# Kernel tuning notes

Measured on AMD Instinct MI355X. Metric: run time of the kernel, lower is better.

Reference implementation:

```python
import jax, jax.numpy as jnp
import numpy as np

BATCH = 1024
M = 64      # N_v measurements
N = 8192    # N_theta unknowns
STEPS = 3   # N_admm_steps
EPS_DIV = 1e-12


def setup_inputs() -> dict:
    key = jax.random.key(0)
    k = jax.random.split(key, 4)
    return {
        "r_n": jax.random.normal(k[0], (BATCH, 2, N), jnp.float32),
        "y": jax.random.normal(k[1], (BATCH, 2, M), jnp.float32),
        "u_in": jax.random.normal(k[2], (BATCH, 2, M), jnp.float32),
        "A": jax.random.normal(k[3], (2, M, N), jnp.float32) / np.sqrt(N).astype(np.float32),
        "log_rho": jnp.zeros((), jnp.float32),                 # rho = 1.0
        "log_epsilon": jnp.asarray(np.log(0.01), jnp.float32), # epsilon = 0.01
    }


def _cmm(Ar, Ai, v):
    # complex matmul A @ v : v [b,2,N] -> [b,2,M]
    vr, vi = v[:, 0], v[:, 1]
    return jnp.stack([vr @ Ar.T - vi @ Ai.T, vi @ Ar.T + vr @ Ai.T], axis=1)


def _chm(Ar, Ai, v):
    # complex conj-transpose matmul A^H @ v : v [b,2,M] -> [b,2,N]
    vr, vi = v[:, 0], v[:, 1]
    return jnp.stack([vr @ Ar + vi @ Ai, vi @ Ar - vr @ Ai], axis=1)


def reference(r_n, y, u_in, A, log_rho, log_epsilon):
    rho = jnp.exp(log_rho)
    epsilon = jnp.exp(log_epsilon)
    Ar, Ai = A[0], A[1]  # [M, N]

    # SMW system matrix: S = (1/rho) I + A A^H, written as real 2Mx2M block matrix.
    # It is constant across ADMM steps (rho fixed within a forward pass).
    I_M = jnp.eye(M, dtype=A.dtype)
    S_r = I_M / (rho + EPS_DIV) + Ar @ Ar.T + Ai @ Ai.T
    S_i = Ai @ Ar.T - Ar @ Ai.T
    S_block = jnp.block([[S_r, -S_i], [S_i, S_r]])  # [2M, 2M]

    x, z, u = r_n, y, u_in
    for _ in range(STEPS):
        # x-update via SMW: x = b - A^H (S^{-1} A b), b = r_n + rho A^H (z - u)
        b = r_n + rho * _chm(Ar, Ai, z - u)          # [b,2,N]
        Ab = _cmm(Ar, Ai, b)                          # [b,2,M]
        R = jnp.concatenate([Ab[:, 0], Ab[:, 1]], axis=1)  # [b,2M]
        sol = jnp.linalg.solve(S_block, R.T)          # [2M, b]
        T = jnp.stack([sol[:M].T, sol[M:].T], axis=1)  # [b,2,M]
        x = b - _chm(Ar, Ai, T)                       # [b,2,N]
        # enforce_real: zero imaginary part; enforce_positivity: clamp real part
        x = jnp.stack([jnp.maximum(x[:, 0], 0.0), jnp.zeros_like(x[:, 0])], axis=1)
        # z-update: project residual onto complex L2 ball of radius epsilon
        Ax = _cmm(Ar, Ai, x)                          # [b,2,M]
        v = Ax + u - y
        nrm = jnp.sqrt(jnp.sum(v * v, axis=(1, 2), keepdims=True))
        z = y + v * jnp.minimum(1.0, epsilon / (nrm + EPS_DIV))
        # dual update
        u = u + Ax - z
    return x, u
```

## Files before the change

kernel.cpp:

```cpp
#include <hip/hip_runtime.h>

#define B_ 1024
#define M_ 64
#define N_ 8192
#define NSG 16
#define NS3 8

typedef __attribute__((ext_vector_type(8))) short bf16x8;
typedef __attribute__((ext_vector_type(4))) float f32x4;

__device__ inline unsigned short f2b(float f) {
    union { float f; unsigned u; } v; v.f = f;
    unsigned r = v.u + 0x7FFFu + ((v.u >> 16) & 1u);
    return (unsigned short)(r >> 16);
}
__device__ inline unsigned rne2(float lo, float hi) {
    union { float f; unsigned u; } a, b; a.f = lo; b.f = hi;
    unsigned x = (a.u + 0x7FFFu + ((a.u >> 16) & 1u)) >> 16;
    unsigned y = (b.u + 0x7FFFu + ((b.u >> 16) & 1u)) >> 16;
    return x | (y << 16);
}
__device__ inline float b2f(unsigned short s) {
    union { unsigned u; float f; } v; v.u = ((unsigned)s) << 16; return v.f;
}
__device__ inline float rl(float v, int l) {
    return __builtin_bit_cast(float, __builtin_amdgcn_readlane(__builtin_bit_cast(int, v), l));
}

__global__ __launch_bounds__(256) void k_cvt(const float* src, unsigned short* dst) {
    size_t i = ((size_t)blockIdx.x * 256 + threadIdx.x) * 8;
    float4 f0 = *(const float4*)(src + i);
    float4 f1 = *(const float4*)(src + i + 4);
    union { bf16x8 v; unsigned u[4]; } r;
    r.u[0] = rne2(f0.x, f0.y); r.u[1] = rne2(f0.z, f0.w);
    r.u[2] = rne2(f1.x, f1.y); r.u[3] = rne2(f1.z, f1.w);
    *(bf16x8*)(dst + i) = r.v;
}

__global__ __launch_bounds__(256) void k_prep(const float* A, unsigned short* Abf,
                                              unsigned short* WgT, unsigned short* ATb) {
    __shared__ float tile[128][65];
    int n0 = blockIdx.x * 64;
    int t = threadIdx.x;
    int nl = t % 64, r0 = t / 64;
#pragma unroll
    for (int it = 0; it < 32; ++it) {
        int row = r0 + it * 4;
        tile[row][nl] = A[(size_t)row * N_ + n0 + nl];
    }
    __syncthreads();
#pragma unroll
    for (int it = 0; it < 32; ++it) {
        int row = r0 + it * 4;
        float v = tile[row][nl];
        unsigned short bv = f2b(v);
        Abf[(size_t)row * N_ + n0 + nl] = bv;
        if (row < 64) {
            WgT[(size_t)row * 16384 + n0 + nl] = bv;
            WgT[(size_t)(64 + row) * 16384 + 8192 + n0 + nl] = bv;
        } else {
            int m = row - 64;
            WgT[(size_t)m * 16384 + 8192 + n0 + nl] = f2b(-v);
            WgT[(size_t)(64 + m) * 16384 + n0 + nl] = bv;
        }
    }
    int o = t % 128, nn0 = t / 128;
#pragma unroll
    for (int it = 0; it < 32; ++it) {
        int nn = nn0 + it * 2;
        ATb[(size_t)(n0 + nn) * 128 + o] = f2b(tile[o][nn]);
    }
}

__global__ __launch_bounds__(256) void k_Sbuild(const float* A, const float* lr,
                                                float* S, float* AAHT) {
    __shared__ float redS[8];
    int bid = blockIdx.x;
    int i = 0, rem = bid;
    while (rem >= 64 - i) { rem -= 64 - i; ++i; }
    int j = i + rem;
    int t = threadIdx.x;
    const float* Ar = A;
    const float* Ai = A + (size_t)M_ * N_;
    const float* ari = Ar + (size_t)i * N_;
    const float* aii = Ai + (size_t)i * N_;
    const float* arj = Ar + (size_t)j * N_;
    const float* aij = Ai + (size_t)j * N_;
    float aR = 0.f, aI = 0.f;
#pragma unroll
    for (int it = 0; it < 8; ++it) {
        int n = it * 1024 + t * 4;
        float4 xr = *(const float4*)(ari + n);
        float4 xi = *(const float4*)(aii + n);
        float4 br = *(const float4*)(arj + n);
        float4 bi = *(const float4*)(aij + n);
        aR += xr.x * br.x + xi.x * bi.x + xr.y * br.y + xi.y * bi.y
            + xr.z * br.z + xi.z * bi.z + xr.w * br.w + xi.w * bi.w;
        aI += xi.x * br.x - xr.x * bi.x + xi.y * br.y - xr.y * bi.y
            + xi.z * br.z - xr.z * bi.z + xi.w * br.w - xr.w * bi.w;
    }
    for (int off = 32; off > 0; off >>= 1) {
        aR += __shfl_down(aR, off, 64);
        aI += __shfl_down(aI, off, 64);
    }
    int lane = t & 63, w = t >> 6;
    if (lane == 0) { redS[w * 2] = aR; redS[w * 2 + 1] = aI; }
    __syncthreads();
    if (t == 0) {
        float R = redS[0] + redS[2] + redS[4] + redS[6];
        float I = redS[1] + redS[3] + redS[5] + redS[7];
        float inv_rho = 1.0f / (expf(lr[0]) + 1e-12f);
        float diag = (i == j) ? inv_rho : 0.f;
        S[((size_t)i * 64 + j) * 2 + 0] = R + diag;
        S[((size_t)i * 64 + j) * 2 + 1] = I;
        AAHT[((size_t)j * 64 + i) * 2 + 0] = R;
        AAHT[((size_t)j * 64 + i) * 2 + 1] = I;
        if (i != j) {
            S[((size_t)j * 64 + i) * 2 + 0] = R;
            S[((size_t)j * 64 + i) * 2 + 1] = -I;
            AAHT[((size_t)i * 64 + j) * 2 + 0] = R;
            AAHT[((size_t)i * 64 + j) * 2 + 1] = -I;
        }
    }
}

__global__ __launch_bounds__(256, 2) void k_Ginv(const unsigned short* rnb,
                                                 const unsigned short* WgT,
                                                 float* Gpart,
                                                 const float* S, float* Wt) {
    int t = threadIdx.x;
    int lane = t & 63;
    if (blockIdx.x == 0) {
        __builtin_amdgcn_s_setprio(1);
        __shared__ float2 Tp[2][4][64];
        int g = t >> 6;
        float mx0,my0,mx1,my1,mx2,my2,mx3,my3,mx4,my4,mx5,my5,mx6,my6,mx7,my7;
        float mx8,my8,mx9,my9,mx10,my10,mx11,my11,mx12,my12,mx13,my13,mx14,my14,mx15,my15;
#define GJ_INIT(J) { int c = 16 * ((J) >> 2) + 4 * g + ((J) & 3);            \
    float2 v = ((const float2*)S)[(size_t)lane * 64 + c];                    \
    mx##J = v.x; my##J = v.y; }
        GJ_INIT(0) GJ_INIT(1) GJ_INIT(2) GJ_INIT(3) GJ_INIT(4) GJ_INIT(5) GJ_INIT(6) GJ_INIT(7)
        GJ_INIT(8) GJ_INIT(9) GJ_INIT(10) GJ_INIT(11) GJ_INIT(12) GJ_INIT(13) GJ_INIT(14) GJ_INIT(15)
#undef GJ_INIT

#define PIV(JA, JB0, JB1, JB2, jj) {                                         \
    int k = p4 + (jj);                                                       \
    float px = rl(mx##JA, k), py = rl(my##JA, k);                            \
    float d = px * px + py * py;                                             \
    float id = 1.0f / d;                                                     \
    float pix = px * id, piy = -py * id;                                     \
    bool isk = (lane == k);                                                  \
    float a   = isk ? 0.f : 1.f;                                             \
    float fpx = isk ? -pix : (mx##JA * pix - my##JA * piy);                  \
    float fpy = isk ? -piy : (mx##JA * piy + my##JA * pix);                  \
    { float sx = rl(mx##JB0, k), sy = rl(my##JB0, k);                        \
      float nx = a * mx##JB0 - (fpx * sx - fpy * sy);                        \
      float ny = a * my##JB0 - (fpx * sy + fpy * sx);                        \
      mx##JB0 = nx; my##JB0 = ny; }                                          \
    { float sx = rl(mx##JB1, k), sy = rl(my##JB1, k);                        \
      float nx = a * mx##JB1 - (fpx * sx - fpy * sy);                        \
      float ny = a * my##JB1 - (fpx * sy + fpy * sx);                        \
      mx##JB1 = nx; my##JB1 = ny; }                                          \
    { float sx = rl(mx##JB2, k), sy = rl(my##JB2, k);                        \
      float nx = a * mx##JB2 - (fpx * sx - fpy * sy);                        \
      float ny = a * my##JB2 - (fpx * sy + fpy * sx);                        \
      mx##JB2 = nx; my##JB2 = ny; }                                          \
    mx##JA = -fpx; my##JA = -fpy; }

#define FACT4(J0, J1, J2, J3) {                                              \
    PIV(J0, J1, J2, J3, 0) PIV(J1, J0, J2, J3, 1)                            \
    PIV(J2, J0, J1, J3, 2) PIV(J3, J0, J1, J2, 3)                            \
    Tp[buf][0][lane] = make_float2(mx##J0, my##J0);                          \
    Tp[buf][1][lane] = make_float2(mx##J1, my##J1);                          \
    Tp[buf][2][lane] = make_float2(mx##J2, my##J2);                          \
    Tp[buf][3][lane] = make_float2(mx##J3, my##J3); }

        for (int p = 0; p < 16; ++p) {
            const int buf = p & 1;
            const int p4  = p * 4;
            const int q   = p >> 2;
            const bool own = (g == (p & 3));
            if (own) {
                switch (q) {
                    case 0:  FACT4(0, 1, 2, 3)     break;
                    case 1:  FACT4(4, 5, 6, 7)     break;
                    case 2:  FACT4(8, 9, 10, 11)   break;
                    default: FACT4(12, 13, 14, 15) break;
                }
            }
            __syncthreads();
            float2 t0 = Tp[buf][0][lane];
            float2 t1 = Tp[buf][1][lane];
            float2 t2 = Tp[buf][2][lane];
            float2 t3 = Tp[buf][3][lane];
            float msk = ((lane >> 2) == p) ? 0.f : 1.f;
            int skipq = own ? q : -1;
#define TRAIL(J) if (((J) >> 2) != skipq) {                                  \
    float s0x = rl(mx##J, p4),     s0y = rl(my##J, p4);                      \
    float s1x = rl(mx##J, p4 + 1), s1y = rl(my##J, p4 + 1);                  \
    float s2x = rl(mx##J, p4 + 2), s2y = rl(my##J, p4 + 2);                  \
    float s3x = rl(mx##J, p4 + 3), s3y = rl(my##J, p4 + 3);                  \
    float ax = msk * mx##J, ay = msk * my##J;                                \
    ax += t0.x * s0x - t0.y * s0y; ay += t0.x * s0y + t0.y * s0x;            \
    ax += t1.x * s1x - t1.y * s1y; ay += t1.x * s1y + t1.y * s1x;            \
    ax += t2.x * s2x - t2.y * s2y; ay += t2.x * s2y + t2.y * s2x;            \
    ax += t3.x * s3x - t3.y * s3y; ay += t3.x * s3y + t3.y * s3x;            \
    mx##J = ax; my##J = ay; }
            TRAIL(0)  TRAIL(1)  TRAIL(2)  TRAIL(3)
            TRAIL(4)  TRAIL(5)  TRAIL(6)  TRAIL(7)
            TRAIL(8)  TRAIL(9)  TRAIL(10) TRAIL(11)
            TRAIL(12) TRAIL(13) TRAIL(14) TRAIL(15)
#undef TRAIL
        }
#undef FACT4
#undef PIV
#define GJ_OUT(J) { int c = 16 * ((J) >> 2) + 4 * g + ((J) & 3);             \
    ((float2*)Wt)[(size_t)c * 64 + lane] = make_float2(mx##J, my##J); }
        GJ_OUT(0) GJ_OUT(1) GJ_OUT(2) GJ_OUT(3) GJ_OUT(4) GJ_OUT(5) GJ_OUT(6) GJ_OUT(7)
        GJ_OUT(8) GJ_OUT(9) GJ_OUT(10) GJ_OUT(11) GJ_OUT(12) GJ_OUT(13) GJ_OUT(14) GJ_OUT(15)
#undef GJ_OUT
        __builtin_amdgcn_s_setprio(0);
    }
    int bx = blockIdx.x;
    int w = t >> 6;
    int l15 = lane & 15;
    int q8 = (lane >> 4) * 8;
    int split = bx & 15;
    int b0 = (bx >> 4) * 16;
    int k0 = split * 1024;
    f32x4 a00 = {}, a01 = {};
    const unsigned short* x0 = rnb + (size_t)(b0 + l15) * 16384 + k0 + q8;
    const unsigned short* w0 = WgT + (size_t)(w * 32 + l15) * 16384 + k0 + q8;
    const unsigned short* w1 = w0 + (size_t)16 * 16384;
#pragma unroll 8
    for (int ks = 0; ks < 32; ++ks) {
        int kk = ks * 32;
        bf16x8 af0 = *(const bf16x8*)(x0 + kk);
        bf16x8 bf0 = *(const bf16x8*)(w0 + kk);
        bf16x8 bf1 = *(const bf16x8*)(w1 + kk);
        a00 = __builtin_amdgcn_mfma_f32_16x16x32_bf16(af0, bf0, a00, 0, 0, 0);
        a01 = __builtin_amdgcn_mfma_f32_16x16x32_bf16(af0, bf1, a01, 0, 0, 0);
    }
    int row = (lane >> 4) * 4;
    size_t base = (size_t)split * (B_ * 128);
    float* g = Gpart + base + (size_t)(b0 + row) * 128 + w * 32 + l15;
#pragma unroll
    for (int r = 0; r < 4; ++r) {
        g[(size_t)r * 128] = a00[r];
        g[(size_t)r * 128 + 16] = a01[r];
    }
}

__global__ __launch_bounds__(256) void k_small12(const float* Gpart, const float* AAHT,
                                                 const float* Wt, const float* zin,
                                                 const float* uin, const float* lr,
                                                 unsigned short* qb) {
    __shared__ float2 AbS[4][64];
    int t = threadIdx.x;
    int m = t & 63;
    int w = __builtin_amdgcn_readfirstlane(t >> 6);
    int b = blockIdx.x * 4 + w;
    float rho = expf(lr[0]);
    float abR = 0.f, abI = 0.f;
    for (int k = 0; k < 64; ++k) {
        float wr = zin[(b * 2 + 0) * 64 + k] - uin[(b * 2 + 0) * 64 + k];
        float wi = zin[(b * 2 + 1) * 64 + k] - uin[(b * 2 + 1) * 64 + k];
        float2 h = *(const float2*)(AAHT + ((size_t)k * 64 + m) * 2);
        abR += wr * h.x - wi * h.y;
        abI += wi * h.x + wr * h.y;
    }
    float gR = 0.f, gI = 0.f;
#pragma unroll
    for (int s = 0; s < NSG; ++s) {
        gR += Gpart[(size_t)s * 131072 + (size_t)b * 128 + m];
        gI += Gpart[(size_t)s * 131072 + (size_t)b * 128 + 64 + m];
    }
    abR = gR + rho * abR;
    abI = gI + rho * abI;
    AbS[w][m] = make_float2(abR, abI);
    __syncthreads();
    float tR = 0.f, tI = 0.f;
    for (int k = 0; k < 64; ++k) {
        float2 Wv = *(const float2*)(Wt + ((size_t)k * 64 + m) * 2);
        float2 ab = AbS[w][k];
        tR += ab.x * Wv.x - ab.y * Wv.y;
        tI += ab.y * Wv.x + ab.x * Wv.y;
    }
    float wr_m = zin[(b * 2 + 0) * 64 + m] - uin[(b * 2 + 0) * 64 + m];
    float wi_m = zin[(b * 2 + 1) * 64 + m] - uin[(b * 2 + 1) * 64 + m];
    qb[(size_t)b * 128 + m] = f2b(rho * wr_m - tR);
    qb[(size_t)b * 128 + 64 + m] = f2b(rho * wi_m - tI);
}

__global__ __launch_bounds__(512, 2) void k_H23(const unsigned short* qb, const unsigned short* ATb,
                                                const unsigned short* rnb, const unsigned short* Abf,
                                                float* out, float* Axpart, int last) {
    __shared__ __align__(16) char lds_buf[8 * 8448];
    int t = threadIdx.x;
    int lane = t & 63;
    int w = t >> 6;
    int l15 = lane & 15;
    int q8 = (lane >> 4) * 8;
    int row = (lane >> 4) * 4;
    int slab = blockIdx.x;
    int b0 = blockIdx.y * 16;
    int n0 = slab * 1024 + w * 128;
    short* xs = (short*)(lds_buf + w * 8448);
    float* rs = (float*)(lds_buf + w * 8448);

    bf16x8 a[4];
    const unsigned short* qrow = qb + (size_t)(b0 + l15) * 128 + q8;
#pragma unroll
    for (int ks = 0; ks < 4; ++ks) a[ks] = *(const bf16x8*)(qrow + ks * 32);
#pragma unroll 2
    for (int nt = 0; nt < 8; ++nt) {
        f32x4 acc = {};
        const unsigned short* bbase = ATb + (size_t)(n0 + nt * 16 + l15) * 128 + q8;
#pragma unroll
        for (int ks = 0; ks < 4; ++ks) {
            bf16x8 bf = *(const bf16x8*)(bbase + ks * 32);
            acc = __builtin_amdgcn_mfma_f32_16x16x32_bf16(a[ks], bf, acc, 0, 0, 0);
        }
        int ncol = n0 + nt * 16 + l15;
        int nloc = nt * 16 + l15;
#pragma unroll
        for (int r = 0; r < 4; ++r) {
            size_t ridx = (size_t)(b0 + row + r) * 16384 + ncol;
            float v = fmaxf(acc[r] + b2f(rnb[ridx]), 0.f);
            if (last) out[ridx] = v;
            xs[(row + r) * 264 + nloc] = (short)f2b(v);
        }
    }
    f32x4 acc8[8] = {};
#pragma unroll
    for (int ks = 0; ks < 4; ++ks) {
        bf16x8 xf = *(const bf16x8*)(xs + l15 * 264 + ks * 32 + q8);
#pragma unroll
        for (int ot = 0; ot < 8; ++ot) {
            const unsigned short* bp = Abf + (size_t)(ot * 16 + l15) * 8192 + n0 + ks * 32 + q8;
            acc8[ot] = __builtin_amdgcn_mfma_f32_16x16x32_bf16(xf, *(const bf16x8*)bp, acc8[ot], 0, 0, 0);
        }
    }
    __syncthreads();
#pragma unroll
    for (int ot = 0; ot < 8; ++ot)
#pragma unroll
        for (int r = 0; r < 4; ++r)
            rs[(row + r) * 132 + ot * 16 + l15] = acc8[ot][r];
    __syncthreads();
#pragma unroll
    for (int e = t; e < 2048; e += 512) {
        int b = e >> 7, o = e & 127;
        float sAx = 0.f;
#pragma unroll
        for (int ww = 0; ww < 8; ++ww)
            sAx += ((const float*)(lds_buf + ww * 8448))[b * 132 + o];
        Axpart[(size_t)slab * 131072 + (size_t)(b0 + b) * 128 + o] = sAx;
    }
    if (last) {
        float4 z4 = make_float4(0.f, 0.f, 0.f, 0.f);
        for (int e = t; e < 4096; e += 512) {
            int bb = e >> 8, nq = e & 255;
            *(float4*)(out + ((size_t)(b0 + bb) * 2 + 1) * N_ + slab * 1024 + nq * 4) = z4;
        }
    }
}

__global__ __launch_bounds__(128) void k_small3(const float* Axpart, const float* uin,
                                                const float* y, const float* le,
                                                float* z, float* u, float* uout, int last) {
    __shared__ float red[2];
    int b = blockIdx.x, t = threadIdx.x;
    size_t idx = (size_t)b * 128 + t;
    float ax = 0.f;
#pragma unroll
    for (int s = 0; s < NS3; ++s) ax += Axpart[(size_t)s * 131072 + idx];
    float uo = uin[idx], yv = y[idx];
    float v = ax + uo - yv;
    float sq = v * v;
    for (int off = 32; off > 0; off >>= 1) sq += __shfl_down(sq, off, 64);
    if ((t & 63) == 0) red[t >> 6] = sq;
    __syncthreads();
    float tot = red[0] + red[1];
    float eps = expf(le[0]);
    float scale = fminf(1.f, eps / (sqrtf(tot) + 1e-12f));
    float zv = yv + v * scale;
    float un = uo + ax - zv;
    z[idx] = zv;
    u[idx] = un;
    if (last) uout[idx] = un;
}

extern "C" void kernel_launch(void* const* d_in, const int* in_sizes, int n_in,
                              void* d_out, int out_size, void* d_ws, size_t ws_size,
                              hipStream_t stream) {
    const float* rn  = (const float*)d_in[0];
    const float* y   = (const float*)d_in[1];
    const float* uin = (const float*)d_in[2];
    const float* A   = (const float*)d_in[3];
    const float* lr  = (const float*)d_in[4];
    const float* le  = (const float*)d_in[5];

    float* out = (float*)d_out;
    float* ws  = (float*)d_ws;

    float* Gpart  = ws;
    float* Axpart = Gpart + (size_t)NSG * 131072;
    float* S      = Axpart + (size_t)NS3 * 131072;
    float* AAHT   = S + 8192;
    float* Wt     = AAHT + 8192;
    float* z      = Wt + 8192;
    float* u      = z + 131072;
    unsigned short* qb  = (unsigned short*)(u + 131072);
    unsigned short* rnb = qb + 131072;
    unsigned short* WgT = rnb + (size_t)B_ * 16384;
    unsigned short* Abf = WgT + 2097152;
    unsigned short* ATb = Abf + 1048576;
    float* uout = out + (size_t)B_ * 2 * N_;

    k_prep<<<128, 256, 0, stream>>>(A, Abf, WgT, ATb);
    k_cvt<<<8192, 256, 0, stream>>>(rn, rnb);
    k_Sbuild<<<2080, 256, 0, stream>>>(A, lr, S, AAHT);
    k_Ginv<<<1024, 256, 0, stream>>>(rnb, WgT, Gpart, S, Wt);

    for (int step = 0; step < 3; ++step) {
        const float* zp = (step == 0) ? y   : z;
        const float* up = (step == 0) ? uin : u;
        int last = (step == 2) ? 1 : 0;
        k_small12<<<256, 256, 0, stream>>>(Gpart, AAHT, Wt, zp, up, lr, qb);
        k_H23<<<dim3(NS3, 64), 512, 0, stream>>>(qb, ATb, rnb, Abf, out, Axpart, last);
        k_small3<<<B_, 128, 0, stream>>>(Axpart, up, y, le, z, u, uout, last);
    }
}
```

Measured before the change: 341.1 us.

## Split small12 reductions across waves and move imag-zeroing into prep kernel

k_small12 now assigns one batch row per block and splits the 64-term k loops and Gpart split sums across four waves, combining partials through LDS. The aim is to cut the serial per-thread latency of that small kernel and raise parallelism. The zero-fill of the output's imaginary half moves out of the last k_H23 call into 2048 extra blocks of k_prep, so the final H23 no longer carries those stores. The cost is extra syncs and LDS traffic in small12, plus a larger prep launch.

```diff
diff --git a/kernel.cpp b/kernel.cpp
--- a/kernel.cpp
+++ b/kernel.cpp
@@ -38,7 +38,18 @@
 }
 
 __global__ __launch_bounds__(256) void k_prep(const float* A, unsigned short* Abf,
-                                              unsigned short* WgT, unsigned short* ATb) {
+                                              unsigned short* WgT, unsigned short* ATb,
+                                              float* out) {
+    if (blockIdx.x >= 128) {
+        int z = blockIdx.x - 128;
+        int fi = z * 4096 + threadIdx.x * 16;
+        int b = fi >> 13;
+        int n = fi & 8191;
+        float4* p = (float4*)(out + (size_t)b * 16384 + 8192 + n);
+        float4 z4 = make_float4(0.f, 0.f, 0.f, 0.f);
+        p[0] = z4; p[1] = z4; p[2] = z4; p[3] = z4;
+        return;
+    }
     __shared__ float tile[128][65];
     int n0 = blockIdx.x * 64;
     int t = threadIdx.x;
@@ -255,41 +266,58 @@
                                                  const float* Wt, const float* zin,
                                                  const float* uin, const float* lr,
                                                  unsigned short* qb) {
-    __shared__ float2 AbS[4][64];
+    __shared__ float2 partA[4][64];
+    __shared__ float2 partB[4][64];
+    __shared__ float2 AbS[64];
     int t = threadIdx.x;
     int m = t & 63;
     int w = __builtin_amdgcn_readfirstlane(t >> 6);
-    int b = blockIdx.x * 4 + w;
+    int b = blockIdx.x;
     float rho = expf(lr[0]);
-    float abR = 0.f, abI = 0.f;
-    for (int k = 0; k < 64; ++k) {
+    float aR = 0.f, aI = 0.f;
+#pragma unroll
+    for (int kk = 0; kk < 16; ++kk) {
+        int k = w * 16 + kk;
         float wr = zin[(b * 2 + 0) * 64 + k] - uin[(b * 2 + 0) * 64 + k];
         float wi = zin[(b * 2 + 1) * 64 + k] - uin[(b * 2 + 1) * 64 + k];
         float2 h = *(const float2*)(AAHT + ((size_t)k * 64 + m) * 2);
-        abR += wr * h.x - wi * h.y;
-        abI += wi * h.x + wr * h.y;
-    }
-    float gR = 0.f, gI = 0.f;
-#pragma unroll
-    for (int s = 0; s < NSG; ++s) {
-        gR += Gpart[(size_t)s * 131072 + (size_t)b * 128 + m];
-        gI += Gpart[(size_t)s * 131072 + (size_t)b * 128 + 64 + m];
-    }
-    abR = gR + rho * abR;
-    abI = gI + rho * abI;
-    AbS[w][m] = make_float2(abR, abI);
+        aR += wr * h.x - wi * h.y;
+        aI += wi * h.x + wr * h.y;
+    }
+    aR *= rho; aI *= rho;
+#pragma unroll
+    for (int s4 = 0; s4 < 4; ++s4) {
+        int s = w * 4 + s4;
+        aR += Gpart[(size_t)s * 131072 + (size_t)b * 128 + m];
+        aI += Gpart[(size_t)s * 131072 + (size_t)b * 128 + 64 + m];
+    }
+    partA[w][m] = make_float2(aR, aI);
+    __syncthreads();
+    if (w == 0) {
+        float2 p0 = partA[0][m], p1 = partA[1][m], p2 = partA[2][m], p3 = partA[3][m];
+        AbS[m] = make_float2(p0.x + p1.x + p2.x + p3.x, p0.y + p1.y + p2.y + p3.y);
+    }
     __syncthreads();
     float tR = 0.f, tI = 0.f;
-    for (int k = 0; k < 64; ++k) {
+#pragma unroll
+    for (int kk = 0; kk < 16; ++kk) {
+        int k = w * 16 + kk;
         float2 Wv = *(const float2*)(Wt + ((size_t)k * 64 + m) * 2);
-        float2 ab = AbS[w][k];
+        float2 ab = AbS[k];
         tR += ab.x * Wv.x - ab.y * Wv.y;
         tI += ab.y * Wv.x + ab.x * Wv.y;
     }
-    float wr_m = zin[(b * 2 + 0) * 64 + m] - uin[(b * 2 + 0) * 64 + m];
-    float wi_m = zin[(b * 2 + 1) * 64 + m] - uin[(b * 2 + 1) * 64 + m];
-    qb[(size_t)b * 128 + m] = f2b(rho * wr_m - tR);
-    qb[(size_t)b * 128 + 64 + m] = f2b(rho * wi_m - tI);
+    partB[w][m] = make_float2(tR, tI);
+    __syncthreads();
+    if (w == 0) {
+        float2 q0 = partB[0][m], q1 = partB[1][m], q2 = partB[2][m], q3 = partB[3][m];
+        float sR = q0.x + q1.x + q2.x + q3.x;
+        float sI = q0.y + q1.y + q2.y + q3.y;
+        float wr_m = zin[(b * 2 + 0) * 64 + m] - uin[(b * 2 + 0) * 64 + m];
+        float wi_m = zin[(b * 2 + 1) * 64 + m] - uin[(b * 2 + 1) * 64 + m];
+        qb[(size_t)b * 128 + m] = f2b(rho * wr_m - sR);
+        qb[(size_t)b * 128 + 64 + m] = f2b(rho * wi_m - sI);
+    }
 }
 
 __global__ __launch_bounds__(512, 2) void k_H23(const unsigned short* qb, const unsigned short* ATb,
@@ -357,13 +385,6 @@
             sAx += ((const float*)(lds_buf + ww * 8448))[b * 132 + o];
         Axpart[(size_t)slab * 131072 + (size_t)(b0 + b) * 128 + o] = sAx;
     }
-    if (last) {
-        float4 z4 = make_float4(0.f, 0.f, 0.f, 0.f);
-        for (int e = t; e < 4096; e += 512) {
-            int bb = e >> 8, nq = e & 255;
-            *(float4*)(out + ((size_t)(b0 + bb) * 2 + 1) * N_ + slab * 1024 + nq * 4) = z4;
-        }
-    }
 }
 
 __global__ __launch_bounds__(128) void k_small3(const float* Axpart, const float* uin,
@@ -418,7 +439,7 @@
     unsigned short* ATb = Abf + 1048576;
     float* uout = out + (size_t)B_ * 2 * N_;
 
-    k_prep<<<128, 256, 0, stream>>>(A, Abf, WgT, ATb);
+    k_prep<<<2176, 256, 0, stream>>>(A, Abf, WgT, ATb, out);
     k_cvt<<<8192, 256, 0, stream>>>(rn, rnb);
     k_Sbuild<<<2080, 256, 0, stream>>>(A, lr, S, AAHT);
     k_Ginv<<<1024, 256, 0, stream>>>(rnb, WgT, Gpart, S, Wt);
@@ -427,7 +448,7 @@
         const float* zp = (step == 0) ? y   : z;
         const float* up = (step == 0) ? uin : u;
         int last = (step == 2) ? 1 : 0;
-        k_small12<<<256, 256, 0, stream>>>(Gpart, AAHT, Wt, zp, up, lr, qb);
+        k_small12<<<B_, 256, 0, stream>>>(Gpart, AAHT, Wt, zp, up, lr, qb);
         k_H23<<<dim3(NS3, 64), 512, 0, stream>>>(qb, ATb, rnb, Abf, out, Axpart, last);
         k_small3<<<B_, 128, 0, stream>>>(Axpart, up, y, le, z, u, uout, last);
     }
```

Result: no change. 340.7 us (-0.1%).
